# Kernel optimization log

Measured on AMD Instinct MI355X. Metric: run time of the kernel, lower is better.

Reference implementation:

```python
import jax, jax.numpy as jnp
import numpy as np

B, S, E, H = 2, 2048, 1024, 16
HD = E // H

def setup_inputs() -> dict:
    key = jax.random.key(0)
    ks = jax.random.split(key, 12)
    q = jax.random.normal(ks[0], (B, S, E), jnp.float32)
    k = jax.random.normal(ks[1], (B, S, E), jnp.float32)
    v = jax.random.normal(ks[2], (B, S, E), jnp.float32)
    # causal mask: 1.0 where attention is disallowed (upper triangle)
    mask = jnp.triu(jnp.ones((S, S), jnp.float32), k=1)[None, None, :, :]
    w = lambda kk: jax.random.normal(kk, (E, E), jnp.float32) * 0.02
    return {
        "q": q, "k": k, "v": v, "mask": mask,
        "Wq": w(ks[3]), "bq": jnp.zeros((E,), jnp.float32),
        "Wk": w(ks[4]), "bk": jnp.zeros((E,), jnp.float32),
        "Wv": w(ks[5]), "bv": jnp.zeros((E,), jnp.float32),
        "Wz": w(ks[6]), "bz": jnp.zeros((E,), jnp.float32),
    }

def _create_heads(x):
    # Faithful to tf.reshape(tf.transpose(x), (B, H, -1, HD)):
    # tf.transpose reverses all dims: [B,S,E] -> [E,S,B], then reshape.
    return jnp.transpose(x, (2, 1, 0)).reshape(B, H, -1, HD)

def reference(q, k, v, mask, Wq, bq, Wk, bk, Wv, bv, Wz, bz):
    qh = _create_heads(q @ Wq + bq)  # (B,H,S,HD)
    kh = _create_heads(k @ Wk + bk)
    vh = _create_heads(v @ Wv + bv)
    qn = qh / jnp.linalg.norm(qh, axis=-1, keepdims=True)
    kn = kh / jnp.linalg.norm(kh, axis=-1, keepdims=True)
    logits = jnp.einsum('bhqd,bhkd->bhqk', qn, kn) * 1000.0
    logits = logits + mask * -1000000000.0
    attn = jax.nn.softmax(logits, axis=-1)  # (B,H,S,S)
    z = jnp.einsum('bhqk,bhkd->bhqd', attn, vh)
    zc = jnp.transpose(z, (0, 2, 1, 3)).reshape(B, -1, E)
    return zc @ Wz + bz, attn
```

## Files before the change

kernel.cpp:

```cpp
#include <hip/hip_runtime.h>
#include <cstdint>
#include <cstddef>


typedef __bf16 bf16x4 __attribute__((ext_vector_type(4)));
typedef __bf16 bf16x8 __attribute__((ext_vector_type(8)));
typedef float floatx4 __attribute__((ext_vector_type(4)));

#define GLOAD_LDS16(g, l)                                                      \
    __builtin_amdgcn_global_load_lds(                                          \
        (const __attribute__((address_space(1))) void*)(g),                    \
        (__attribute__((address_space(3))) void*)(l), 16, 0, 0)

__global__ __launch_bounds__(256) void split_a(
    const float* __restrict__ x0, const float* __restrict__ x1,
    const float* __restrict__ x2, __bf16* __restrict__ ApBase)
{
    const float* X = blockIdx.z == 0 ? x0 : (blockIdx.z == 1 ? x1 : x2);
    __bf16* Ap = ApBase + (size_t)blockIdx.z * (4096ull * 2048);
    const int idx = blockIdx.x * 256 + threadIdx.x;
    const int r = idx >> 8;
    const int c = (idx & 255) * 4;
    float4 t = *(const float4*)(X + (size_t)r * 1024 + c);
    bf16x4 hi, lo;
    hi[0] = (__bf16)t.x; lo[0] = (__bf16)(t.x - (float)hi[0]);
    hi[1] = (__bf16)t.y; lo[1] = (__bf16)(t.y - (float)hi[1]);
    hi[2] = (__bf16)t.z; lo[2] = (__bf16)(t.z - (float)hi[2]);
    hi[3] = (__bf16)t.w; lo[3] = (__bf16)(t.w - (float)hi[3]);
    *(bf16x4*)(Ap + (size_t)r * 2048 + c) = hi;
    *(bf16x4*)(Ap + (size_t)r * 2048 + 1024 + c) = lo;
}

__global__ __launch_bounds__(256) void split_bt(
    const float* __restrict__ w0, const float* __restrict__ w1,
    const float* __restrict__ w2, __bf16* __restrict__ dstBase, size_t dstStride)
{
    const float* W = blockIdx.z == 0 ? w0 : (blockIdx.z == 1 ? w1 : w2);
    __bf16* Bp = dstBase + (size_t)blockIdx.z * dstStride;
    __shared__ float tile[64][65];
    const int tid = (int)threadIdx.x;
    const int k0 = blockIdx.y * 64, n0 = blockIdx.x * 64;
    #pragma unroll
    for (int p = 0; p < 4; ++p) {
        int kr = p * 16 + (tid >> 4);
        float4 t = *(const float4*)(W + (size_t)(k0 + kr) * 1024 + n0 + (tid & 15) * 4);
        tile[kr][(tid & 15) * 4 + 0] = t.x; tile[kr][(tid & 15) * 4 + 1] = t.y;
        tile[kr][(tid & 15) * 4 + 2] = t.z; tile[kr][(tid & 15) * 4 + 3] = t.w;
    }
    __syncthreads();
    const int nr = tid >> 2, kc = (tid & 3) * 16;
    bf16x8 hi0, hi1, lo0, lo1;
    #pragma unroll
    for (int j = 0; j < 8; ++j) {
        float x = tile[kc + j][nr];
        __bf16 h = (__bf16)x; hi0[j] = h; lo0[j] = (__bf16)(x - (float)h);
        float y = tile[kc + 8 + j][nr];
        __bf16 g = (__bf16)y; hi1[j] = g; lo1[j] = (__bf16)(y - (float)g);
    }
    __bf16* row = Bp + (size_t)(n0 + nr) * 2048;
    *(bf16x8*)(row + k0 + kc)          = hi0;
    *(bf16x8*)(row + k0 + kc + 8)      = hi1;
    *(bf16x8*)(row + 1024 + k0 + kc)     = lo0;
    *(bf16x8*)(row + 1024 + k0 + kc + 8) = lo1;
}

__global__ __launch_bounds__(256) void gemm_split(
    const __bf16* __restrict__ Ap0, size_t aSlice, int aStride,
    const __bf16* __restrict__ Bp0, size_t bSlice,
    const float* __restrict__ b0, const float* __restrict__ b1,
    const float* __restrict__ b2, float* __restrict__ Out0,
    int transposeOut, int chunksQK, int chunksV)
{
    const int z = blockIdx.z;
    const int nch = (z == 2) ? chunksV : chunksQK;
    const __bf16* Ap = Ap0 + (size_t)z * aSlice;
    const __bf16* Bp = Bp0 + (size_t)z * bSlice;
    const float* bias = z == 0 ? b0 : (z == 1 ? b1 : b2);
    float* Out = Out0 + (size_t)z * (4096ull * 1024);

    __shared__ __bf16 As[2 * 128 * 32];
    __shared__ __bf16 Bs[2 * 128 * 32];

    const int tid = (int)threadIdx.x;
    const int wave = tid >> 6, lane = tid & 63;
    const int quad = lane >> 4, tl = lane & 15;
    const int m0 = blockIdx.y * 128, n0 = blockIdx.x * 128;
    const int waveM = wave >> 1, waveN = wave & 1;

    floatx4 acc[4][4];
    #pragma unroll
    for (int i = 0; i < 4; ++i)
        #pragma unroll
        for (int j = 0; j < 4; ++j)
            acc[i][j] = (floatx4){0.f, 0.f, 0.f, 0.f};

    const int sRow  = (wave << 4) + (lane >> 2);
    const int sColB = (lane & 3) << 4;
    auto* AsL = (__attribute__((address_space(3))) char*)As;
    auto* BsL = (__attribute__((address_space(3))) char*)Bs;
    const int ldsOff = wave * 1024;

    for (int k0 = 0; k0 < 1024; k0 += 32) {
        __syncthreads();
        #pragma unroll
        for (int i = 0; i < 2; ++i) {
            GLOAD_LDS16((const char*)(Ap + (size_t)(m0 + i*64 + sRow) * aStride + k0) + sColB,
                        AsL + i * 4096 + ldsOff);
            GLOAD_LDS16((const char*)(Bp + (size_t)(n0 + i*64 + sRow) * 2048 + k0) + sColB,
                        BsL + i * 4096 + ldsOff);
            if (nch > 1) {
                GLOAD_LDS16((const char*)(Ap + 1024 + (size_t)(m0 + i*64 + sRow) * aStride + k0) + sColB,
                            AsL + 8192 + i * 4096 + ldsOff);
                GLOAD_LDS16((const char*)(Bp + 1024 + (size_t)(n0 + i*64 + sRow) * 2048 + k0) + sColB,
                            BsL + 8192 + i * 4096 + ldsOff);
            }
        }
        __syncthreads();

        bf16x8 ah[4], bh[4], al[4], bl[4];
        #pragma unroll
        for (int mt = 0; mt < 4; ++mt)
            ah[mt] = *(const bf16x8*)(As + (waveM*64 + mt*16 + tl) * 32 + quad * 8);
        #pragma unroll
        for (int nt = 0; nt < 4; ++nt)
            bh[nt] = *(const bf16x8*)(Bs + (waveN*64 + nt*16 + tl) * 32 + quad * 8);
        #pragma unroll
        for (int mt = 0; mt < 4; ++mt)
            #pragma unroll
            for (int nt = 0; nt < 4; ++nt)
                acc[mt][nt] = __builtin_amdgcn_mfma_f32_16x16x32_bf16(
                    ah[mt], bh[nt], acc[mt][nt], 0, 0, 0);
        if (nch > 1) {
            #pragma unroll
            for (int mt = 0; mt < 4; ++mt)
                al[mt] = *(const bf16x8*)(As + 4096 + (waveM*64 + mt*16 + tl) * 32 + quad * 8);
            #pragma unroll
            for (int mt = 0; mt < 4; ++mt)
                #pragma unroll
                for (int nt = 0; nt < 4; ++nt)
                    acc[mt][nt] = __builtin_amdgcn_mfma_f32_16x16x32_bf16(
                        al[mt], bh[nt], acc[mt][nt], 0, 0, 0);
        }
        if (nch > 2) {
            #pragma unroll
            for (int nt = 0; nt < 4; ++nt)
                bl[nt] = *(const bf16x8*)(Bs + 4096 + (waveN*64 + nt*16 + tl) * 32 + quad * 8);
            #pragma unroll
            for (int mt = 0; mt < 4; ++mt)
                #pragma unroll
                for (int nt = 0; nt < 4; ++nt)
                    acc[mt][nt] = __builtin_amdgcn_mfma_f32_16x16x32_bf16(
                        ah[mt], bl[nt], acc[mt][nt], 0, 0, 0);
        }
    }

    if (transposeOut) {
        #pragma unroll
        for (int nt = 0; nt < 4; ++nt) {
            const int e = n0 + waveN * 64 + nt * 16 + tl;
            const float bb = bias[e];
            #pragma unroll
            for (int mt = 0; mt < 4; ++mt) {
                floatx4 v = acc[mt][nt] + bb;
                *(floatx4*)(Out + (size_t)e * 4096 + m0 + waveM * 64 + mt * 16 + quad * 4) = v;
            }
        }
    } else {
        #pragma unroll
        for (int mt = 0; mt < 4; ++mt) {
            const int rbase = m0 + waveM * 64 + mt * 16 + quad * 4;
            #pragma unroll
            for (int nt = 0; nt < 4; ++nt) {
                const int e = n0 + waveN * 64 + nt * 16 + tl;
                const float bb = bias[e];
                #pragma unroll
                for (int reg = 0; reg < 4; ++reg)
                    Out[(size_t)(rbase + reg) * 1024 + e] = acc[mt][nt][reg] + bb;
            }
        }
    }
}

__global__ __launch_bounds__(256) void gather_qk(
    const float* __restrict__ PT, __bf16* __restrict__ Outp)
{
    const int tid  = (int)threadIdx.x;
    const int lane = tid & 63;
    const int vec  = blockIdx.x * 4 + (tid >> 6);
    const int head = vec >> 11;
    const int sp   = vec & 2047;
    const int c    = (head >> 4) * 512 + (head & 15) * 32 + (sp >> 6);
    const int src  = (lane & 1) * 2048 + (sp & 63) * 32 + (lane >> 1);
    float v = PT[(size_t)c * 4096 + src];
    float ss = v * v;
    #pragma unroll
    for (int mk = 32; mk >= 1; mk >>= 1) ss += __shfl_xor(ss, mk);
    v = v / sqrtf(ss);
    __bf16 h = (__bf16)v;
    Outp[(size_t)vec * 128 + lane]      = h;
    Outp[(size_t)vec * 128 + 64 + lane] = (__bf16)(v - (float)h);
}

__global__ __launch_bounds__(256) void v_transpose(
    const float* __restrict__ PTv, __bf16* __restrict__ Vt)
{
    const int head = blockIdx.y, st = blockIdx.x;
    const int tid = (int)threadIdx.x;
    const int c = (head >> 4) * 512 + (head & 15) * 32 + st;
    const float* __restrict__ row = PTv + (size_t)c * 4096;

    __shared__ float tile[64][65];
    #pragma unroll
    for (int i = 0; i < 4; ++i) {
        int o = i * 1024 + tid * 4;
        float4 t = *(const float4*)(row + o);
        float vals[4] = {t.x, t.y, t.z, t.w};
        #pragma unroll
        for (int e = 0; e < 4; ++e) {
            int oo = o + e;
            int d  = ((oo & 2047) & 31) * 2 + (oo >> 11);
            int sl = (oo & 2047) >> 5;
            tile[sl][d] = vals[e];
        }
    }
    __syncthreads();

    const int d = tid >> 2, jb = (tid & 3) * 16;
    bf16x8 h0, h1;
    #pragma unroll
    for (int j = 0; j < 8; ++j) {
        h0[j] = (__bf16)tile[jb + j][d];
        h1[j] = (__bf16)tile[jb + 8 + j][d];
    }
    size_t bh = ((size_t)head * 64 + d) * 2048 + st * 64 + jb;
    *(bf16x8*)(Vt + bh)     = h0;
    *(bf16x8*)(Vt + bh + 8) = h1;
}

__global__ __launch_bounds__(512, 4) void attn_mfma(
    const __bf16* __restrict__ Qp, const __bf16* __restrict__ Kp,
    const __bf16* __restrict__ Vt, float* __restrict__ Attn,
    __bf16* __restrict__ Az)
{
    const int flat = (int)blockIdx.x;
    const int head = flat & 31;
    const int it   = 15 - (flat >> 5);
    const int tid = (int)threadIdx.x;
    const int w = tid >> 6, lane = tid & 63;
    const int quad = lane >> 4, tl = lane & 15;
    const int t7 = tl & 7;
    const int i0 = it * 128;
    const int jtmax = 2 * it + 1;
    const int wrowMax = i0 + w * 16 + 15;
    const int wdiag   = (i0 + w * 16) >> 6;

    const __bf16* __restrict__ Qh = Qp + ((size_t)head * 2048 + i0) * 128;
    const __bf16* __restrict__ Kh = Kp + (size_t)head * 2048 * 128;
    const __bf16* __restrict__ Vh = Vt + (size_t)head * 64 * 2048;
    float* __restrict__ Ah = Attn + (size_t)head * ((size_t)2048 * 2048);

    __shared__ __bf16 kb[64 * 128];
    __shared__ __bf16 vt[64 * 64];
    __shared__ __bf16 ps[8][16 * 72];
    __bf16* psw = ps[w];
    auto* kbL = (__attribute__((address_space(3))) char*)kb;
    auto* vtL = (__attribute__((address_space(3))) char*)vt;

    const char* kSrc[2];
    #pragma unroll
    for (int i = 0; i < 2; ++i) {
        int d  = i * 512 + tid;
        int rK = d >> 4, cK = (d & 15) ^ (rK & 7);
        kSrc[i] = (const char*)(Kh + (size_t)rK * 128) + cK * 16;
    }
    const char* vSrc;
    {
        int rV = tid >> 3, cV = (tid & 7) ^ (rV & 7);
        vSrc = (const char*)(Vh + (size_t)rV * 2048) + cV * 16;
    }
    const int ok0 = ((quad)      ^ t7) * 8;
    const int ok1 = ((quad + 4)  ^ t7) * 8;
    const int ok2 = ((quad + 8)  ^ t7) * 8;
    const int ok3 = ((quad + 12) ^ t7) * 8;

    const __bf16* qrow = Qh + (size_t)(w * 16 + tl) * 128;
    bf16x8 qhi0 = *(const bf16x8*)(qrow + quad * 8);
    bf16x8 qhi1 = *(const bf16x8*)(qrow + 32 + quad * 8);
    bf16x8 qlo0 = *(const bf16x8*)(qrow + 64 + quad * 8);
    bf16x8 qlo1 = *(const bf16x8*)(qrow + 96 + quad * 8);

    for (int jt = jtmax + 1; jt < 32; ++jt) {
        float4 z4 = make_float4(0.f, 0.f, 0.f, 0.f);
        #pragma unroll
        for (int g = 0; g < 4; ++g)
            *(float4*)(Ah + (size_t)(i0 + w * 16 + g * 4 + quad) * 2048
                          + jt * 64 + tl * 4) = z4;
    }

    float m[4], l[4];
    #pragma unroll
    for (int r = 0; r < 4; ++r) { m[r] = -3.0e38f; l[r] = 0.0f; }

    for (int jt = 0; jt <= jtmax; ++jt) {
        __syncthreads();
        #pragma unroll
        for (int i = 0; i < 2; ++i)
            GLOAD_LDS16(kSrc[i] + (size_t)jt * 16384, kbL + i * 8192 + w * 1024);
        __syncthreads();
        if (jt * 64 > wrowMax) continue;

        floatx4 S[4];
        #pragma unroll
        for (int sub = 0; sub < 4; ++sub) {
            const __bf16* kr = kb + (sub * 16 + tl) * 128;
            bf16x8 khi0 = *(const bf16x8*)(kr + ok0);
            bf16x8 khi1 = *(const bf16x8*)(kr + ok1);
            bf16x8 klo0 = *(const bf16x8*)(kr + ok2);
            bf16x8 klo1 = *(const bf16x8*)(kr + ok3);
            floatx4 s = (floatx4){0.f, 0.f, 0.f, 0.f};
            s = __builtin_amdgcn_mfma_f32_16x16x32_bf16(qhi0, khi0, s, 0, 0, 0);
            s = __builtin_amdgcn_mfma_f32_16x16x32_bf16(qhi1, khi1, s, 0, 0, 0);
            s = __builtin_amdgcn_mfma_f32_16x16x32_bf16(qhi0, klo0, s, 0, 0, 0);
            s = __builtin_amdgcn_mfma_f32_16x16x32_bf16(qhi1, klo1, s, 0, 0, 0);
            s = __builtin_amdgcn_mfma_f32_16x16x32_bf16(qlo0, khi0, s, 0, 0, 0);
            s = __builtin_amdgcn_mfma_f32_16x16x32_bf16(qlo1, khi1, s, 0, 0, 0);
            S[sub] = s;
        }
        const bool diag = (jt == wdiag);
        #pragma unroll
        for (int reg = 0; reg < 4; ++reg) {
            const int irow = w * 16 + quad * 4 + reg;
            float sl[4];
            #pragma unroll
            for (int sub = 0; sub < 4; ++sub) {
                float lv = S[sub][reg] * 1000.0f;
                if (diag && (jt * 64 + sub * 16 + tl > i0 + irow)) lv = -1.0e9f;
                sl[sub] = lv;
            }
            float mt = fmaxf(fmaxf(sl[0], sl[1]), fmaxf(sl[2], sl[3]));
            float mn = fmaxf(m[reg], mt);
            l[reg] = l[reg] * __expf(m[reg] - mn)
                   + __expf(sl[0]-mn) + __expf(sl[1]-mn)
                   + __expf(sl[2]-mn) + __expf(sl[3]-mn);
            m[reg] = mn;
        }
    }

    #pragma unroll
    for (int reg = 0; reg < 4; ++reg) {
        #pragma unroll
        for (int mk = 8; mk >= 1; mk >>= 1) {
            float mo = __shfl_xor(m[reg], mk);
            float lo = __shfl_xor(l[reg], mk);
            float mn = fmaxf(m[reg], mo);
            l[reg] = l[reg] * __expf(m[reg] - mn) + lo * __expf(mo - mn);
            m[reg] = mn;
        }
    }
    float inv_l[4];
    #pragma unroll
    for (int reg = 0; reg < 4; ++reg) inv_l[reg] = 1.0f / l[reg];

    floatx4 zacc[4];
    #pragma unroll
    for (int t = 0; t < 4; ++t) zacc[t] = (floatx4){0.f, 0.f, 0.f, 0.f};

    for (int jt = 0; jt <= jtmax; ++jt) {
        __syncthreads();
        #pragma unroll
        for (int i = 0; i < 2; ++i)
            GLOAD_LDS16(kSrc[i] + (size_t)jt * 16384, kbL + i * 8192 + w * 1024);
        GLOAD_LDS16(vSrc + (size_t)jt * 128, vtL + w * 1024);
        __syncthreads();

        if (jt * 64 > wrowMax) {
            float4 z4 = make_float4(0.f, 0.f, 0.f, 0.f);
            #pragma unroll
            for (int g = 0; g < 4; ++g)
                *(float4*)(Ah + (size_t)(i0 + w * 16 + g * 4 + quad) * 2048
                              + jt * 64 + tl * 4) = z4;
            continue;
        }

        floatx4 S[4];
        #pragma unroll
        for (int sub = 0; sub < 4; ++sub) {
            const __bf16* kr = kb + (sub * 16 + tl) * 128;
            bf16x8 khi0 = *(const bf16x8*)(kr + ok0);
            bf16x8 khi1 = *(const bf16x8*)(kr + ok1);
            bf16x8 klo0 = *(const bf16x8*)(kr + ok2);
            bf16x8 klo1 = *(const bf16x8*)(kr + ok3);
            floatx4 s = (floatx4){0.f, 0.f, 0.f, 0.f};
            s = __builtin_amdgcn_mfma_f32_16x16x32_bf16(qhi0, khi0, s, 0, 0, 0);
            s = __builtin_amdgcn_mfma_f32_16x16x32_bf16(qhi1, khi1, s, 0, 0, 0);
            s = __builtin_amdgcn_mfma_f32_16x16x32_bf16(qhi0, klo0, s, 0, 0, 0);
            s = __builtin_amdgcn_mfma_f32_16x16x32_bf16(qhi1, klo1, s, 0, 0, 0);
            s = __builtin_amdgcn_mfma_f32_16x16x32_bf16(qlo0, khi0, s, 0, 0, 0);
            s = __builtin_amdgcn_mfma_f32_16x16x32_bf16(qlo1, khi1, s, 0, 0, 0);
            S[sub] = s;
        }
        const bool diag = (jt == wdiag);
        #pragma unroll
        for (int reg = 0; reg < 4; ++reg) {
            const int irow = w * 16 + quad * 4 + reg;
            #pragma unroll
            for (int sub = 0; sub < 4; ++sub) {
                float lv = S[sub][reg] * 1000.0f;
                if (diag && (jt * 64 + sub * 16 + tl > i0 + irow)) lv = -1.0e9f;
                float p = __expf(lv - m[reg]) * inv_l[reg];
                psw[(quad * 4 + reg) * 72 + sub * 16 + tl] = (__bf16)p;
            }
        }
        __asm__ volatile("s_waitcnt lgkmcnt(0)" ::: "memory");

        #pragma unroll
        for (int g = 0; g < 4; ++g) {
            bf16x4 pv = *(const bf16x4*)(psw + (g * 4 + quad) * 72 + tl * 4);
            float4 f = make_float4((float)pv[0], (float)pv[1],
                                   (float)pv[2], (float)pv[3]);
            *(float4*)(Ah + (size_t)(i0 + w * 16 + g * 4 + quad) * 2048
                          + jt * 64 + tl * 4) = f;
        }

        bf16x8 p0 = *(const bf16x8*)(psw + tl * 72 + quad * 8);
        bf16x8 p1 = *(const bf16x8*)(psw + tl * 72 + 32 + quad * 8);

        #pragma unroll
        for (int t = 0; t < 4; ++t) {
            const __bf16* vh0 = vt + (t * 16 + tl) * 64;
            bf16x8 vhi0 = *(const bf16x8*)(vh0 + ok0);
            bf16x8 vhi1 = *(const bf16x8*)(vh0 + ok1);
            zacc[t] = __builtin_amdgcn_mfma_f32_16x16x32_bf16(p0, vhi0, zacc[t], 0, 0, 0);
            zacc[t] = __builtin_amdgcn_mfma_f32_16x16x32_bf16(p1, vhi1, zacc[t], 0, 0, 0);
        }
    }

    const int b = head >> 4, h = head & 15;
    #pragma unroll
    for (int reg = 0; reg < 4; ++reg) {
        const size_t R = (size_t)b * 2048 + i0 + w * 16 + quad * 4 + reg;
        #pragma unroll
        for (int t = 0; t < 4; ++t)
            Az[R * 1024 + h * 64 + t * 16 + tl] = (__bf16)zacc[t][reg];
    }
}

extern "C" void kernel_launch(void* const* d_in, const int* in_sizes, int n_in,
                              void* d_out, int out_size, void* d_ws, size_t ws_size,
                              hipStream_t stream) {
    (void)in_sizes; (void)n_in; (void)out_size;
    const float* q  = (const float*)d_in[0];
    const float* k  = (const float*)d_in[1];
    const float* v  = (const float*)d_in[2];
    const float* Wq = (const float*)d_in[4];  const float* bq = (const float*)d_in[5];
    const float* Wk = (const float*)d_in[6];  const float* bk = (const float*)d_in[7];
    const float* Wv = (const float*)d_in[8];  const float* bv = (const float*)d_in[9];
    const float* Wz = (const float*)d_in[10]; const float* bz = (const float*)d_in[11];

    float* out0 = (float*)d_out;
    float* attn = out0 + 4194304;

    float*  PT0 = attn;
    __bf16* Ap0 = (__bf16*)(attn + 12582912);
    __bf16* Bp0 = (__bf16*)(attn + 12582912 + 12582912);

    __bf16* Bpz = (__bf16*)d_in[4];

    __bf16 *Qp, *Kp, *Vtp, *Az;
    if (ws_size >= (size_t)50331648) {
        __bf16* ws = (__bf16*)d_ws;
        Qp = ws; Kp = ws + 8388608; Vtp = ws + 16777216; Az = ws + 20971520;
    } else {
        Qp = (__bf16*)d_in[0]; Kp = (__bf16*)d_in[1]; Vtp = (__bf16*)d_in[2];
        Az = (__bf16*)d_ws;
    }

    split_a <<<dim3(4096, 1, 3), 256, 0, stream>>>(q, k, v, Ap0);
    split_bt<<<dim3(16, 16, 3), 256, 0, stream>>>(Wq, Wk, Wv, Bp0, 1024ull*2048);

    gemm_split<<<dim3(8, 32, 3), 256, 0, stream>>>(
        Ap0, 4096ull*2048, 2048, Bp0, 1024ull*2048,
        bq, bk, bv, PT0, 1, 3, 1);

    gather_qk  <<<16384, 256, 0, stream>>>(PT0,           Qp);
    gather_qk  <<<16384, 256, 0, stream>>>(PT0 + 4194304, Kp);
    v_transpose<<<dim3(32, 32), 256, 0, stream>>>(PT0 + 8388608, Vtp);

    split_bt<<<dim3(16, 16, 1), 256, 0, stream>>>(Wz, Wz, Wz, Bpz, 0);

    attn_mfma<<<dim3(512), 512, 0, stream>>>(Qp, Kp, Vtp, attn, Az);

    gemm_split<<<dim3(8, 32, 1), 256, 0, stream>>>(
        Az, 0, 1024, Bpz, 0,
        bz, bz, bz, out0, 0, 1, 1);
}
```

Measured before the change: 833.3 us.

## Fuse prep and gather launches and double-buffer K/V tiles in attention

Merges the activation and weight bf16 split kernels into one launch, and the Q/K gather and V transpose into another, cutting launch count and serialization gaps. In the attention kernel, K and V tiles are double-buffered in shared memory so the next tile's global-to-LDS load overlaps the current tile's compute, with one barrier per iteration instead of two. The row-max/sum softmax pass is reworked into a per-element online update fused into the score loop, which uses more exp calls. Double buffering doubles the K/V LDS footprint, which may lower occupancy, and the Wz split buffer moves into the workspace when it is large enough.

```diff
diff --git a/kernel.cpp b/kernel.cpp
--- a/kernel.cpp
+++ b/kernel.cpp
@@ -12,40 +12,50 @@
         (const __attribute__((address_space(1))) void*)(g),                    \
         (__attribute__((address_space(3))) void*)(l), 16, 0, 0)
 
-__global__ __launch_bounds__(256) void split_a(
+__global__ __launch_bounds__(256) void prep(
     const float* __restrict__ x0, const float* __restrict__ x1,
-    const float* __restrict__ x2, __bf16* __restrict__ ApBase)
+    const float* __restrict__ x2, __bf16* __restrict__ ApBase,
+    const float* __restrict__ w0, const float* __restrict__ w1,
+    const float* __restrict__ w2, const float* __restrict__ w3,
+    __bf16* __restrict__ Bp0, __bf16* __restrict__ BpzDst, int nW)
 {
-    const float* X = blockIdx.z == 0 ? x0 : (blockIdx.z == 1 ? x1 : x2);
-    __bf16* Ap = ApBase + (size_t)blockIdx.z * (4096ull * 2048);
-    const int idx = blockIdx.x * 256 + threadIdx.x;
-    const int r = idx >> 8;
-    const int c = (idx & 255) * 4;
-    float4 t = *(const float4*)(X + (size_t)r * 1024 + c);
-    bf16x4 hi, lo;
-    hi[0] = (__bf16)t.x; lo[0] = (__bf16)(t.x - (float)hi[0]);
-    hi[1] = (__bf16)t.y; lo[1] = (__bf16)(t.y - (float)hi[1]);
-    hi[2] = (__bf16)t.z; lo[2] = (__bf16)(t.z - (float)hi[2]);
-    hi[3] = (__bf16)t.w; lo[3] = (__bf16)(t.w - (float)hi[3]);
-    *(bf16x4*)(Ap + (size_t)r * 2048 + c) = hi;
-    *(bf16x4*)(Ap + (size_t)r * 2048 + 1024 + c) = lo;
-}
-
-__global__ __launch_bounds__(256) void split_bt(
-    const float* __restrict__ w0, const float* __restrict__ w1,
-    const float* __restrict__ w2, __bf16* __restrict__ dstBase, size_t dstStride)
-{
-    const float* W = blockIdx.z == 0 ? w0 : (blockIdx.z == 1 ? w1 : w2);
-    __bf16* Bp = dstBase + (size_t)blockIdx.z * dstStride;
+    const int flat = (int)blockIdx.x;
+    const int tid = (int)threadIdx.x;
+
+    if (flat < 12288) {
+        const int z = flat >> 12;
+        const int bx = flat & 4095;
+        const float* X = z == 0 ? x0 : (z == 1 ? x1 : x2);
+        __bf16* Ap = ApBase + (size_t)z * (4096ull * 2048);
+        const int idx = bx * 256 + tid;
+        const int r = idx >> 8;
+        const int c = (idx & 255) * 4;
+        float4 t = *(const float4*)(X + (size_t)r * 1024 + c);
+        bf16x4 hi, lo;
+        hi[0] = (__bf16)t.x; lo[0] = (__bf16)(t.x - (float)hi[0]);
+        hi[1] = (__bf16)t.y; lo[1] = (__bf16)(t.y - (float)hi[1]);
+        hi[2] = (__bf16)t.z; lo[2] = (__bf16)(t.z - (float)hi[2]);
+        hi[3] = (__bf16)t.w; lo[3] = (__bf16)(t.w - (float)hi[3]);
+        *(bf16x4*)(Ap + (size_t)r * 2048 + c) = hi;
+        *(bf16x4*)(Ap + (size_t)r * 2048 + 1024 + c) = lo;
+        return;
+    }
+
+    const int t = flat - 12288;
+    const int slice = t >> 8;
+    if (slice >= nW) return;
+    const int idx = t & 255;
+    const float* W = slice == 0 ? w0 : (slice == 1 ? w1 : (slice == 2 ? w2 : w3));
+    __bf16* Bp = slice < 3 ? (Bp0 + (size_t)slice * (1024ull * 2048)) : BpzDst;
+
     __shared__ float tile[64][65];
-    const int tid = (int)threadIdx.x;
-    const int k0 = blockIdx.y * 64, n0 = blockIdx.x * 64;
+    const int k0 = (idx >> 4) * 64, n0 = (idx & 15) * 64;
     #pragma unroll
     for (int p = 0; p < 4; ++p) {
         int kr = p * 16 + (tid >> 4);
-        float4 t = *(const float4*)(W + (size_t)(k0 + kr) * 1024 + n0 + (tid & 15) * 4);
-        tile[kr][(tid & 15) * 4 + 0] = t.x; tile[kr][(tid & 15) * 4 + 1] = t.y;
-        tile[kr][(tid & 15) * 4 + 2] = t.z; tile[kr][(tid & 15) * 4 + 3] = t.w;
+        float4 v = *(const float4*)(W + (size_t)(k0 + kr) * 1024 + n0 + (tid & 15) * 4);
+        tile[kr][(tid & 15) * 4 + 0] = v.x; tile[kr][(tid & 15) * 4 + 1] = v.y;
+        tile[kr][(tid & 15) * 4 + 2] = v.z; tile[kr][(tid & 15) * 4 + 3] = v.w;
     }
     __syncthreads();
     const int nr = tid >> 2, kc = (tid & 3) * 16;
@@ -58,8 +68,38 @@
         __bf16 g = (__bf16)y; hi1[j] = g; lo1[j] = (__bf16)(y - (float)g);
     }
     __bf16* row = Bp + (size_t)(n0 + nr) * 2048;
-    *(bf16x8*)(row + k0 + kc)          = hi0;
-    *(bf16x8*)(row + k0 + kc + 8)      = hi1;
+    *(bf16x8*)(row + k0 + kc)            = hi0;
+    *(bf16x8*)(row + k0 + kc + 8)        = hi1;
+    *(bf16x8*)(row + 1024 + k0 + kc)     = lo0;
+    *(bf16x8*)(row + 1024 + k0 + kc + 8) = lo1;
+}
+
+__global__ __launch_bounds__(256) void split_bt1(
+    const float* __restrict__ W, __bf16* __restrict__ Bp)
+{
+    __shared__ float tile[64][65];
+    const int tid = (int)threadIdx.x;
+    const int k0 = blockIdx.y * 64, n0 = blockIdx.x * 64;
+    #pragma unroll
+    for (int p = 0; p < 4; ++p) {
+        int kr = p * 16 + (tid >> 4);
+        float4 v = *(const float4*)(W + (size_t)(k0 + kr) * 1024 + n0 + (tid & 15) * 4);
+        tile[kr][(tid & 15) * 4 + 0] = v.x; tile[kr][(tid & 15) * 4 + 1] = v.y;
+        tile[kr][(tid & 15) * 4 + 2] = v.z; tile[kr][(tid & 15) * 4 + 3] = v.w;
+    }
+    __syncthreads();
+    const int nr = tid >> 2, kc = (tid & 3) * 16;
+    bf16x8 hi0, hi1, lo0, lo1;
+    #pragma unroll
+    for (int j = 0; j < 8; ++j) {
+        float x = tile[kc + j][nr];
+        __bf16 h = (__bf16)x; hi0[j] = h; lo0[j] = (__bf16)(x - (float)h);
+        float y = tile[kc + 8 + j][nr];
+        __bf16 g = (__bf16)y; hi1[j] = g; lo1[j] = (__bf16)(y - (float)g);
+    }
+    __bf16* row = Bp + (size_t)(n0 + nr) * 2048;
+    *(bf16x8*)(row + k0 + kc)            = hi0;
+    *(bf16x8*)(row + k0 + kc + 8)        = hi1;
     *(bf16x8*)(row + 1024 + k0 + kc)     = lo0;
     *(bf16x8*)(row + 1024 + k0 + kc + 8) = lo1;
 }
@@ -181,31 +221,37 @@
     }
 }
 
-__global__ __launch_bounds__(256) void gather_qk(
-    const float* __restrict__ PT, __bf16* __restrict__ Outp)
+__global__ __launch_bounds__(256) void gather_all(
+    const float* __restrict__ PT0, __bf16* __restrict__ Qp,
+    __bf16* __restrict__ Kp, __bf16* __restrict__ Vt)
 {
-    const int tid  = (int)threadIdx.x;
-    const int lane = tid & 63;
-    const int vec  = blockIdx.x * 4 + (tid >> 6);
-    const int head = vec >> 11;
-    const int sp   = vec & 2047;
-    const int c    = (head >> 4) * 512 + (head & 15) * 32 + (sp >> 6);
-    const int src  = (lane & 1) * 2048 + (sp & 63) * 32 + (lane >> 1);
-    float v = PT[(size_t)c * 4096 + src];
-    float ss = v * v;
-    #pragma unroll
-    for (int mk = 32; mk >= 1; mk >>= 1) ss += __shfl_xor(ss, mk);
-    v = v / sqrtf(ss);
-    __bf16 h = (__bf16)v;
-    Outp[(size_t)vec * 128 + lane]      = h;
-    Outp[(size_t)vec * 128 + 64 + lane] = (__bf16)(v - (float)h);
-}
-
-__global__ __launch_bounds__(256) void v_transpose(
-    const float* __restrict__ PTv, __bf16* __restrict__ Vt)
-{
-    const int head = blockIdx.y, st = blockIdx.x;
+    const int flat = (int)blockIdx.x;
     const int tid = (int)threadIdx.x;
+
+    if (flat < 32768) {
+        const float* PT = flat < 16384 ? PT0 : (PT0 + 4194304);
+        __bf16* Outp = flat < 16384 ? Qp : Kp;
+        const int bx = flat & 16383;
+        const int lane = tid & 63;
+        const int vec  = bx * 4 + (tid >> 6);
+        const int head = vec >> 11;
+        const int sp   = vec & 2047;
+        const int c    = (head >> 4) * 512 + (head & 15) * 32 + (sp >> 6);
+        const int src  = (lane & 1) * 2048 + (sp & 63) * 32 + (lane >> 1);
+        float v = PT[(size_t)c * 4096 + src];
+        float ss = v * v;
+        #pragma unroll
+        for (int mk = 32; mk >= 1; mk >>= 1) ss += __shfl_xor(ss, mk);
+        v = v / sqrtf(ss);
+        __bf16 h = (__bf16)v;
+        Outp[(size_t)vec * 128 + lane]      = h;
+        Outp[(size_t)vec * 128 + 64 + lane] = (__bf16)(v - (float)h);
+        return;
+    }
+
+    const int t = flat - 32768;
+    const int st = t & 31, head = t >> 5;
+    const float* PTv = PT0 + 8388608;
     const int c = (head >> 4) * 512 + (head & 15) * 32 + st;
     const float* __restrict__ row = PTv + (size_t)c * 4096;
 
@@ -213,8 +259,8 @@
     #pragma unroll
     for (int i = 0; i < 4; ++i) {
         int o = i * 1024 + tid * 4;
-        float4 t = *(const float4*)(row + o);
-        float vals[4] = {t.x, t.y, t.z, t.w};
+        float4 v4 = *(const float4*)(row + o);
+        float vals[4] = {v4.x, v4.y, v4.z, v4.w};
         #pragma unroll
         for (int e = 0; e < 4; ++e) {
             int oo = o + e;
@@ -253,18 +299,19 @@
     const int jtmax = 2 * it + 1;
     const int wrowMax = i0 + w * 16 + 15;
     const int wdiag   = (i0 + w * 16) >> 6;
+    const int irowBase = w * 16 + quad * 4;
 
     const __bf16* __restrict__ Qh = Qp + ((size_t)head * 2048 + i0) * 128;
     const __bf16* __restrict__ Kh = Kp + (size_t)head * 2048 * 128;
     const __bf16* __restrict__ Vh = Vt + (size_t)head * 64 * 2048;
     float* __restrict__ Ah = Attn + (size_t)head * ((size_t)2048 * 2048);
 
-    __shared__ __bf16 kb[64 * 128];
-    __shared__ __bf16 vt[64 * 64];
+    __shared__ __bf16 kb[2][64 * 128];
+    __shared__ __bf16 vt[2][64 * 64];
     __shared__ __bf16 ps[8][16 * 72];
     __bf16* psw = ps[w];
-    auto* kbL = (__attribute__((address_space(3))) char*)kb;
-    auto* vtL = (__attribute__((address_space(3))) char*)vt;
+    auto* kbL = (__attribute__((address_space(3))) char*)&kb[0][0];
+    auto* vtL = (__attribute__((address_space(3))) char*)&vt[0][0];
 
     const char* kSrc[2];
     #pragma unroll
@@ -301,18 +348,26 @@
     #pragma unroll
     for (int r = 0; r < 4; ++r) { m[r] = -3.0e38f; l[r] = 0.0f; }
 
+    #pragma unroll
+    for (int i = 0; i < 2; ++i)
+        GLOAD_LDS16(kSrc[i], kbL + i * 8192 + w * 1024);
+
     for (int jt = 0; jt <= jtmax; ++jt) {
+        const int cur = jt & 1;
         __syncthreads();
-        #pragma unroll
-        for (int i = 0; i < 2; ++i)
-            GLOAD_LDS16(kSrc[i] + (size_t)jt * 16384, kbL + i * 8192 + w * 1024);
-        __syncthreads();
+        if (jt < jtmax) {
+            #pragma unroll
+            for (int i = 0; i < 2; ++i)
+                GLOAD_LDS16(kSrc[i] + (size_t)(jt + 1) * 16384,
+                            kbL + (cur ^ 1) * 16384 + i * 8192 + w * 1024);
+        }
         if (jt * 64 > wrowMax) continue;
 
-        floatx4 S[4];
+        const __bf16* kbuf = &kb[cur][0];
+        const bool diag = (jt == wdiag);
         #pragma unroll
         for (int sub = 0; sub < 4; ++sub) {
-            const __bf16* kr = kb + (sub * 16 + tl) * 128;
+            const __bf16* kr = kbuf + (sub * 16 + tl) * 128;
             bf16x8 khi0 = *(const bf16x8*)(kr + ok0);
             bf16x8 khi1 = *(const bf16x8*)(kr + ok1);
             bf16x8 klo0 = *(const bf16x8*)(kr + ok2);
@@ -324,25 +379,15 @@
             s = __builtin_amdgcn_mfma_f32_16x16x32_bf16(qhi1, klo1, s, 0, 0, 0);
             s = __builtin_amdgcn_mfma_f32_16x16x32_bf16(qlo0, khi0, s, 0, 0, 0);
             s = __builtin_amdgcn_mfma_f32_16x16x32_bf16(qlo1, khi1, s, 0, 0, 0);
-            S[sub] = s;
-        }
-        const bool diag = (jt == wdiag);
-        #pragma unroll
-        for (int reg = 0; reg < 4; ++reg) {
-            const int irow = w * 16 + quad * 4 + reg;
-            float sl[4];
-            #pragma unroll
-            for (int sub = 0; sub < 4; ++sub) {
-                float lv = S[sub][reg] * 1000.0f;
-                if (diag && (jt * 64 + sub * 16 + tl > i0 + irow)) lv = -1.0e9f;
-                sl[sub] = lv;
+            const int col = jt * 64 + sub * 16 + tl;
+            #pragma unroll
+            for (int reg = 0; reg < 4; ++reg) {
+                float lv = s[reg] * 1000.0f;
+                if (diag && (col > i0 + irowBase + reg)) lv = -1.0e9f;
+                float mn = fmaxf(m[reg], lv);
+                l[reg] = l[reg] * __expf(m[reg] - mn) + __expf(lv - mn);
+                m[reg] = mn;
             }
-            float mt = fmaxf(fmaxf(sl[0], sl[1]), fmaxf(sl[2], sl[3]));
-            float mn = fmaxf(m[reg], mt);
-            l[reg] = l[reg] * __expf(m[reg] - mn)
-                   + __expf(sl[0]-mn) + __expf(sl[1]-mn)
-                   + __expf(sl[2]-mn) + __expf(sl[3]-mn);
-            m[reg] = mn;
         }
     }
 
@@ -365,13 +410,22 @@
     #pragma unroll
     for (int t = 0; t < 4; ++t) zacc[t] = (floatx4){0.f, 0.f, 0.f, 0.f};
 
+    #pragma unroll
+    for (int i = 0; i < 2; ++i)
+        GLOAD_LDS16(kSrc[i], kbL + i * 8192 + w * 1024);
+    GLOAD_LDS16(vSrc, vtL + w * 1024);
+
     for (int jt = 0; jt <= jtmax; ++jt) {
+        const int cur = jt & 1;
         __syncthreads();
-        #pragma unroll
-        for (int i = 0; i < 2; ++i)
-            GLOAD_LDS16(kSrc[i] + (size_t)jt * 16384, kbL + i * 8192 + w * 1024);
-        GLOAD_LDS16(vSrc + (size_t)jt * 128, vtL + w * 1024);
-        __syncthreads();
+        if (jt < jtmax) {
+            #pragma unroll
+            for (int i = 0; i < 2; ++i)
+                GLOAD_LDS16(kSrc[i] + (size_t)(jt + 1) * 16384,
+                            kbL + (cur ^ 1) * 16384 + i * 8192 + w * 1024);
+            GLOAD_LDS16(vSrc + (size_t)(jt + 1) * 128,
+                        vtL + (cur ^ 1) * 8192 + w * 1024);
+        }
 
         if (jt * 64 > wrowMax) {
             float4 z4 = make_float4(0.f, 0.f, 0.f, 0.f);
@@ -382,10 +436,12 @@
             continue;
         }
 
-        floatx4 S[4];
+        const __bf16* kbuf = &kb[cur][0];
+        const __bf16* vbuf = &vt[cur][0];
+        const bool diag = (jt == wdiag);
         #pragma unroll
         for (int sub = 0; sub < 4; ++sub) {
-            const __bf16* kr = kb + (sub * 16 + tl) * 128;
+            const __bf16* kr = kbuf + (sub * 16 + tl) * 128;
             bf16x8 khi0 = *(const bf16x8*)(kr + ok0);
             bf16x8 khi1 = *(const bf16x8*)(kr + ok1);
             bf16x8 klo0 = *(const bf16x8*)(kr + ok2);
@@ -397,16 +453,11 @@
             s = __builtin_amdgcn_mfma_f32_16x16x32_bf16(qhi1, klo1, s, 0, 0, 0);
             s = __builtin_amdgcn_mfma_f32_16x16x32_bf16(qlo0, khi0, s, 0, 0, 0);
             s = __builtin_amdgcn_mfma_f32_16x16x32_bf16(qlo1, khi1, s, 0, 0, 0);
-            S[sub] = s;
-        }
-        const bool diag = (jt == wdiag);
-        #pragma unroll
-        for (int reg = 0; reg < 4; ++reg) {
-            const int irow = w * 16 + quad * 4 + reg;
-            #pragma unroll
-            for (int sub = 0; sub < 4; ++sub) {
-                float lv = S[sub][reg] * 1000.0f;
-                if (diag && (jt * 64 + sub * 16 + tl > i0 + irow)) lv = -1.0e9f;
+            const int col = jt * 64 + sub * 16 + tl;
+            #pragma unroll
+            for (int reg = 0; reg < 4; ++reg) {
+                float lv = s[reg] * 1000.0f;
+                if (diag && (col > i0 + irowBase + reg)) lv = -1.0e9f;
                 float p = __expf(lv - m[reg]) * inv_l[reg];
                 psw[(quad * 4 + reg) * 72 + sub * 16 + tl] = (__bf16)p;
             }
@@ -424,10 +475,9 @@
 
         bf16x8 p0 = *(const bf16x8*)(psw + tl * 72 + quad * 8);
         bf16x8 p1 = *(const bf16x8*)(psw + tl * 72 + 32 + quad * 8);
-
         #pragma unroll
         for (int t = 0; t < 4; ++t) {
-            const __bf16* vh0 = vt + (t * 16 + tl) * 64;
+            const __bf16* vh0 = vbuf + (t * 16 + tl) * 64;
             bf16x8 vhi0 = *(const bf16x8*)(vh0 + ok0);
             bf16x8 vhi1 = *(const bf16x8*)(vh0 + ok1);
             zacc[t] = __builtin_amdgcn_mfma_f32_16x16x32_bf16(p0, vhi0, zacc[t], 0, 0, 0);
@@ -464,29 +514,32 @@
     __bf16* Ap0 = (__bf16*)(attn + 12582912);
     __bf16* Bp0 = (__bf16*)(attn + 12582912 + 12582912);
 
-    __bf16* Bpz = (__bf16*)d_in[4];
-
-    __bf16 *Qp, *Kp, *Vtp, *Az;
-    if (ws_size >= (size_t)50331648) {
+    __bf16 *Qp, *Kp, *Vtp, *Az, *Bpz;
+    const bool bigWs = ws_size >= (size_t)54525952;
+    if (bigWs) {
         __bf16* ws = (__bf16*)d_ws;
         Qp = ws; Kp = ws + 8388608; Vtp = ws + 16777216; Az = ws + 20971520;
+        Bpz = ws + 25165824;
     } else {
         Qp = (__bf16*)d_in[0]; Kp = (__bf16*)d_in[1]; Vtp = (__bf16*)d_in[2];
         Az = (__bf16*)d_ws;
-    }
-
-    split_a <<<dim3(4096, 1, 3), 256, 0, stream>>>(q, k, v, Ap0);
-    split_bt<<<dim3(16, 16, 3), 256, 0, stream>>>(Wq, Wk, Wv, Bp0, 1024ull*2048);
+        Bpz = (__bf16*)d_in[4];
+    }
+
+    if (bigWs) {
+        prep<<<dim3(12288 + 4 * 256), 256, 0, stream>>>(
+            q, k, v, Ap0, Wq, Wk, Wv, Wz, Bp0, Bpz, 4);
+    } else {
+        prep<<<dim3(12288 + 3 * 256), 256, 0, stream>>>(
+            q, k, v, Ap0, Wq, Wk, Wv, Wz, Bp0, nullptr, 3);
+        split_bt1<<<dim3(16, 16), 256, 0, stream>>>(Wz, Bpz);
+    }
 
     gemm_split<<<dim3(8, 32, 3), 256, 0, stream>>>(
         Ap0, 4096ull*2048, 2048, Bp0, 1024ull*2048,
         bq, bk, bv, PT0, 1, 3, 1);
 
-    gather_qk  <<<16384, 256, 0, stream>>>(PT0,           Qp);
-    gather_qk  <<<16384, 256, 0, stream>>>(PT0 + 4194304, Kp);
-    v_transpose<<<dim3(32, 32), 256, 0, stream>>>(PT0 + 8388608, Vtp);
-
-    split_bt<<<dim3(16, 16, 1), 256, 0, stream>>>(Wz, Wz, Wz, Bpz, 0);
+    gather_all<<<dim3(33792), 256, 0, stream>>>(PT0, Qp, Kp, Vtp);
 
     attn_mfma<<<dim3(512), 512, 0, stream>>>(Qp, Kp, Vtp, attn, Az);
 
```

Result: no change. 821.9 us (-1.4%).
